# Kernel tuning notes

Hardware: AMD Instinct MI355X
Metric: run time of the kernel (lower is better)

## Reference

```python
import jax, jax.numpy as jnp
import numpy as np

N_NODES = 20000
N_EDGE_TYPES = 5
N_EDGES = 64000
IN_C, HID_C, OUT_C = 2048, 1024, 512


def setup_inputs() -> dict:
    key = jax.random.key(0)
    ks = jax.random.split(key, 12)
    s = 0.02
    return {
        "x": jax.random.normal(ks[0], (N_NODES, IN_C), jnp.float32),
        "edges": jax.random.randint(ks[1], (N_EDGE_TYPES, 2, N_EDGES), 0, N_NODES, dtype=jnp.int32),
        # SAGEConv weights, stacked over the 5 edge types. lin_l (neighbor agg, with bias), lin_r (root, no bias)
        "Wl1": jax.random.normal(ks[2], (N_EDGE_TYPES, HID_C, IN_C), jnp.float32) * s,
        "bl1": jnp.zeros((N_EDGE_TYPES, HID_C), jnp.float32),
        "Wr1": jax.random.normal(ks[3], (N_EDGE_TYPES, HID_C, IN_C), jnp.float32) * s,
        "Wl2": jax.random.normal(ks[4], (N_EDGE_TYPES, HID_C, HID_C), jnp.float32) * s,
        "bl2": jnp.zeros((N_EDGE_TYPES, HID_C), jnp.float32),
        "Wr2": jax.random.normal(ks[5], (N_EDGE_TYPES, HID_C, HID_C), jnp.float32) * s,
        "Wl3": jax.random.normal(ks[6], (N_EDGE_TYPES, OUT_C, HID_C), jnp.float32) * s,
        "bl3": jnp.zeros((N_EDGE_TYPES, OUT_C), jnp.float32),
        "Wr3": jax.random.normal(ks[7], (N_EDGE_TYPES, OUT_C, HID_C), jnp.float32) * s,
        "attn": jnp.ones((N_EDGE_TYPES,), jnp.float32),
    }


def sage_conv(h, src, dst, Wl, bl, Wr):
    # PyG SAGEConv(aggr='mean'): out = lin_l(mean_{j in N(i)} h_j) + lin_r(h_i)
    msg_sum = jax.ops.segment_sum(h[src], dst, num_segments=N_NODES)  # [N, C_in]
    deg = jax.ops.segment_sum(jnp.ones(src.shape, h.dtype), dst, num_segments=N_NODES)
    agg = msg_sum / jnp.maximum(deg, 1.0)[:, None]
    return agg @ Wl.T + bl + h @ Wr.T


def reference(x, edges, Wl1, bl1, Wr1, Wl2, bl2, Wr2, Wl3, bl3, Wr3, attn):
    outs = []
    for i in range(N_EDGE_TYPES):  # fixed small set of edge types
        src, dst = edges[i, 0], edges[i, 1]
        h = jax.nn.relu(sage_conv(x, src, dst, Wl1[i], bl1[i], Wr1[i]))
        h = jax.nn.relu(sage_conv(h, src, dst, Wl2[i], bl2[i], Wr2[i]))
        h = sage_conv(h, src, dst, Wl3[i], bl3[i], Wr3[i])  # no relu on final layer
        outs.append(h)
    w = jax.nn.softmax(attn)  # softmax-weighted combine over edge types
    combined = sum(w[i] * outs[i] for i in range(N_EDGE_TYPES))
    # F.normalize(p=2, dim=1, eps=1e-12)
    norm = jnp.linalg.norm(combined, axis=1, keepdims=True)
    return combined / jnp.maximum(norm, 1e-12)
```

## Files before the change

### kernel.cpp

```cpp
#include <hip/hip_runtime.h>
#include <hip/hip_bf16.h>
#include <stdint.h>

#define N_NODES   20000
#define MPAD      20224
#define N_TYPES   5
#define N_EDGES   64000
#define IN_C      2048
#define HID_C     1024
#define OUT_C     512

typedef __attribute__((ext_vector_type(8))) short short8;
typedef __attribute__((ext_vector_type(4))) float f32x4;

__device__ __forceinline__ unsigned short f2b(float f) {
  union { float f; uint32_t u; } c; c.f = f;
  uint32_t u = c.u;
  u += 0x7FFFu + ((u >> 16) & 1u);
  return (unsigned short)(u >> 16);
}
__device__ __forceinline__ float b2f(unsigned short h) {
  union { uint32_t u; float f; } c; c.u = ((uint32_t)h) << 16; return c.f;
}
__device__ __forceinline__ void gload_lds16(const void* g, void* l) {
  __builtin_amdgcn_global_load_lds((__attribute__((address_space(1))) void*)g,
                                   (__attribute__((address_space(3))) void*)l,
                                   16, 0, 0);
}

__global__ __launch_bounds__(64) void softmax5_k(const float* __restrict__ attn, float* __restrict__ w) {
  if (threadIdx.x == 0) {
    float m = attn[0];
    for (int i = 1; i < N_TYPES; ++i) m = fmaxf(m, attn[i]);
    float e[N_TYPES], s = 0.f;
    for (int i = 0; i < N_TYPES; ++i) { e[i] = expf(attn[i] - m); s += e[i]; }
    for (int i = 0; i < N_TYPES; ++i) w[i] = e[i] / s;
  }
}

__global__ __launch_bounds__(256) void zero_int_k(int* __restrict__ p, int n) {
  int i = blockIdx.x * 256 + threadIdx.x;
  if (i < n) p[i] = 0;
}

__global__ __launch_bounds__(256) void hist_k(const int* __restrict__ edges, int* __restrict__ deg) {
  int t = blockIdx.x * 256 + threadIdx.x;
  if (t < N_TYPES * N_EDGES) {
    int ty = t / N_EDGES, e = t - ty * N_EDGES;
    int dst = edges[ty * 2 * N_EDGES + N_EDGES + e];
    atomicAdd(&deg[ty * N_NODES + dst], 1);
  }
}

__global__ __launch_bounds__(256) void scan_k(const int* __restrict__ deg, int* __restrict__ rowptr,
                                              int* __restrict__ cursor) {
  int ty = blockIdx.x;
  const int* d = deg + ty * N_NODES;
  int* rp = rowptr + ty * (N_NODES + 1);
  int* cu = cursor + ty * N_NODES;
  __shared__ int sh[256];
  __shared__ int s_carry;
  int tid = threadIdx.x;
  if (tid == 0) s_carry = 0;
  __syncthreads();
  for (int base = 0; base < N_NODES; base += 256) {
    int i = base + tid;
    int v = (i < N_NODES) ? d[i] : 0;
    sh[tid] = v; __syncthreads();
    for (int off = 1; off < 256; off <<= 1) {
      int t2 = (tid >= off) ? sh[tid - off] : 0;
      __syncthreads();
      sh[tid] += t2;
      __syncthreads();
    }
    int incl = sh[tid];
    int c = s_carry;
    if (i < N_NODES) { rp[i] = c + incl - v; cu[i] = c + incl - v; }
    __syncthreads();
    if (tid == 255) s_carry = c + incl;
    __syncthreads();
  }
  if (tid == 0) rp[N_NODES] = s_carry;
}

__global__ __launch_bounds__(256) void scatter_k(const int* __restrict__ edges, int* __restrict__ cursor,
                                                 int* __restrict__ colidx) {
  int t = blockIdx.x * 256 + threadIdx.x;
  if (t < N_TYPES * N_EDGES) {
    int ty = t / N_EDGES, e = t - ty * N_EDGES;
    int src = edges[ty * 2 * N_EDGES + e];
    int dst = edges[ty * 2 * N_EDGES + N_EDGES + e];
    int pos = atomicAdd(&cursor[ty * N_NODES + dst], 1);
    colidx[ty * N_EDGES + pos] = src;
  }
}

__global__ __launch_bounds__(256) void cvt_x_k(const float* __restrict__ x, unsigned short* __restrict__ xb) {
  int i = blockIdx.x * 256 + threadIdx.x;
  int row = i >> 9;
  int c4 = (i & 511) << 2;
  if (row >= MPAD) return;
  ushort4 o;
  if (row < N_NODES) {
    float4 v = *(const float4*)(x + (size_t)row * IN_C + c4);
    o.x = f2b(v.x); o.y = f2b(v.y); o.z = f2b(v.z); o.w = f2b(v.w);
  } else { o.x = 0; o.y = 0; o.z = 0; o.w = 0; }
  *(ushort4*)(xb + (size_t)row * IN_C + c4) = o;
}

__global__ __launch_bounds__(256) void cvt_wcat_k(const float* __restrict__ s,
                                                  unsigned short* __restrict__ d,
                                                  int C, int K4, int rowoff) {
  int i = blockIdx.x * 256 + threadIdx.x;
  int total = N_TYPES * C * K4;
  if (i >= total) return;
  int k4 = i % K4;
  int rr = (i / K4) % C;
  int it = i / (C * K4);
  float4 v = ((const float4*)s)[i];
  ushort4 o; o.x = f2b(v.x); o.y = f2b(v.y); o.z = f2b(v.z); o.w = f2b(v.w);
  ((ushort4*)d)[((size_t)it * 2 * C + rowoff + rr) * K4 + k4] = o;
}

template<int NSIZE, int KSIZE>
__global__ __launch_bounds__(512, 2) void gemm_k(
    const unsigned short* __restrict__ Abase, size_t aS,
    const unsigned short* __restrict__ Wbase,
    unsigned short* __restrict__ PQ) {
  constexpr int NT = KSIZE / 32;
  constexpr int MT = MPAD / 256;
  constexpr int NB = NSIZE / 256;
  __shared__ unsigned short As[4][8192];
  __shared__ unsigned short Bs[4][8192];
  const int tid = threadIdx.x;
  const int lane = tid & 63;
  const int wave = tid >> 6;
  const int wm = wave >> 2, wn = wave & 3;

  const int nwg = gridDim.x;
  const int flat = blockIdx.x;
  const int q8 = nwg >> 3, r8 = nwg & 7;
  const int xcd = flat & 7, idx = flat >> 3;
  const int wg = (xcd < r8) ? (xcd * (q8 + 1) + idx) : (r8 * (q8 + 1) + (xcd - r8) * q8 + idx);
  const int itl = wg / (MT * NB);
  const int rem = wg % (MT * NB);
  const int row0 = (rem / NB) * 256;
  const int col0 = (rem % NB) * 256;

  const unsigned short* A = Abase + (size_t)itl * aS;
  const unsigned short* W = Wbase + (size_t)itl * NSIZE * KSIZE;

  const int sR = lane >> 3;
  const int su = (lane & 7) ^ (sR & 7);
  const int srow = 2 * sR + (su >> 2);
  const int selem = (su & 3) * 8;

  const int fr = lane & 15, k16 = lane >> 4;
  int aoff[8], boff[4];
#pragma unroll
  for (int m = 0; m < 8; ++m) {
    int r = wm * 128 + m * 16 + fr;
    aoff[m] = (((r >> 1) << 7) + ((r & 1) << 6) + (k16 << 4)) ^ (((r >> 1) & 7) << 4);
  }
#pragma unroll
  for (int n = 0; n < 4; ++n) {
    int r = wn * 64 + n * 16 + fr;
    boff[n] = (((r >> 1) << 7) + ((r & 1) << 6) + (k16 << 4)) ^ (((r >> 1) & 7) << 4);
  }

  auto stageA = [&](int t) {
    int s = t & 3; int kb = t * 32;
#pragma unroll
    for (int j = 0; j < 2; ++j) {
      int reg = wave + 8 * j;
      gload_lds16(A + (size_t)(row0 + reg * 16 + srow) * KSIZE + kb + selem, &As[s][reg * 512]);
    }
  };
  auto stageB = [&](int t) {
    int s = t & 3; int kb = t * 32;
#pragma unroll
    for (int j = 0; j < 2; ++j) {
      int reg = wave + 8 * j;
      gload_lds16(W + (size_t)(col0 + reg * 16 + srow) * KSIZE + kb + selem, &Bs[s][reg * 512]);
    }
  };

  f32x4 acc[8][4];
#pragma unroll
  for (int m = 0; m < 8; ++m)
#pragma unroll
    for (int n = 0; n < 4; ++n) acc[m][n] = (f32x4)(0.f);

  stageA(0); stageB(0);
  stageA(1); stageB(1);
  stageA(2); stageB(2);

  for (int t = 0; t < NT; ++t) {
    if (t < NT - 2)       asm volatile("s_waitcnt vmcnt(8)" ::: "memory");
    else if (t == NT - 2) asm volatile("s_waitcnt vmcnt(4)" ::: "memory");
    else                  asm volatile("s_waitcnt vmcnt(0)" ::: "memory");
    __builtin_amdgcn_s_barrier();
    __builtin_amdgcn_sched_barrier(0);
    const int slot = t & 3;
    const char* pa = (const char*)As[slot];
    const char* pb = (const char*)Bs[slot];
    short8 bf[4];
#pragma unroll
    for (int n = 0; n < 4; ++n) bf[n] = *(const short8*)(pb + boff[n]);
    short8 af[4];
#pragma unroll
    for (int m = 0; m < 4; ++m) af[m] = *(const short8*)(pa + aoff[m]);
    if (t + 3 < NT) stageA(t + 3);
    __builtin_amdgcn_s_setprio(1);
#pragma unroll
    for (int m = 0; m < 4; ++m)
#pragma unroll
      for (int n = 0; n < 4; ++n)
        acc[m][n] = __builtin_amdgcn_mfma_f32_16x16x32_bf16(af[m], bf[n], acc[m][n], 0, 0, 0);
    __builtin_amdgcn_s_setprio(0);
    __builtin_amdgcn_s_barrier();
    __builtin_amdgcn_sched_barrier(0);
#pragma unroll
    for (int m = 0; m < 4; ++m) af[m] = *(const short8*)(pa + aoff[m + 4]);
    if (t + 3 < NT) stageB(t + 3);
    __builtin_amdgcn_s_setprio(1);
#pragma unroll
    for (int m = 0; m < 4; ++m)
#pragma unroll
      for (int n = 0; n < 4; ++n)
        acc[m + 4][n] = __builtin_amdgcn_mfma_f32_16x16x32_bf16(af[m], bf[n], acc[m + 4][n], 0, 0, 0);
    __builtin_amdgcn_s_setprio(0);
  }

  const int erow = (lane >> 4) * 4;
  const int ecol = lane & 15;
  unsigned short* Op = PQ + (size_t)itl * MPAD * NSIZE;
#pragma unroll
  for (int m = 0; m < 8; ++m) {
#pragma unroll
    for (int n = 0; n < 4; ++n) {
      int gcol = col0 + wn * 64 + n * 16 + ecol;
#pragma unroll
      for (int r = 0; r < 4; ++r) {
        int grow = row0 + wm * 128 + m * 16 + erow + r;
        Op[(size_t)grow * NSIZE + gcol] = f2b(acc[m][n][r]);
      }
    }
  }
}

__global__ __launch_bounds__(256) void combine12_k(const unsigned short* __restrict__ PQ,
                                                   unsigned short* __restrict__ Hn,
                                                   const float* __restrict__ bl,
                                                   const int* __restrict__ rowptr,
                                                   const int* __restrict__ colidx, int it0) {
  constexpr int C = HID_C;
  int itl = blockIdx.x / MPAD;
  int node = blockIdx.x % MPAD;
  int it = it0 + itl;
  int tid = threadIdx.x;
  unsigned short* hp = Hn + ((size_t)itl * MPAD + node) * C + tid * 4;
  if (node >= N_NODES) {
    ushort4 z; z.x = 0; z.y = 0; z.z = 0; z.w = 0;
    *(ushort4*)hp = z;
    return;
  }
  const unsigned short* Pb = PQ + (size_t)itl * MPAD * 2 * C;
  const int* rp = rowptr + (size_t)it * (N_NODES + 1);
  const int* ci = colidx + (size_t)it * N_EDGES;
  int beg = rp[node], end = rp[node + 1];
  float a0 = 0.f, a1 = 0.f, a2 = 0.f, a3 = 0.f;
  for (int e = beg; e < end; ++e) {
    int src = ci[e];
    ushort4 u = *(const ushort4*)(Pb + (size_t)src * 2 * C + tid * 4);
    a0 += b2f(u.x); a1 += b2f(u.y); a2 += b2f(u.z); a3 += b2f(u.w);
  }
  float inv = (end > beg) ? 1.f / (float)(end - beg) : 0.f;
  a0 *= inv; a1 *= inv; a2 *= inv; a3 *= inv;
  ushort4 qv = *(const ushort4*)(Pb + (size_t)node * 2 * C + C + tid * 4);
  float4 bv = *(const float4*)(bl + (size_t)it * C + tid * 4);
  ushort4 o;
  o.x = f2b(fmaxf(a0 + b2f(qv.x) + bv.x, 0.f));
  o.y = f2b(fmaxf(a1 + b2f(qv.y) + bv.y, 0.f));
  o.z = f2b(fmaxf(a2 + b2f(qv.z) + bv.z, 0.f));
  o.w = f2b(fmaxf(a3 + b2f(qv.w) + bv.w, 0.f));
  *(ushort4*)hp = o;
}

__global__ __launch_bounds__(128) void combine3_k(const unsigned short* __restrict__ PQ,
                                                  const float* __restrict__ bl3,
                                                  const float* __restrict__ wsm,
                                                  const int* __restrict__ rowptr,
                                                  const int* __restrict__ colidx,
                                                  float* __restrict__ out, int it0, int nb, int acc) {
  int node = blockIdx.x;
  int tid = threadIdx.x;
  float s0 = 0.f, s1 = 0.f, s2 = 0.f, s3 = 0.f;
  for (int itl = 0; itl < nb; ++itl) {
    int it = it0 + itl;
    const unsigned short* Pb = PQ + (size_t)itl * MPAD * 1024;
    const int* rp = rowptr + (size_t)it * (N_NODES + 1);
    const int* ci = colidx + (size_t)it * N_EDGES;
    int beg = rp[node], end = rp[node + 1];
    float a0 = 0.f, a1 = 0.f, a2 = 0.f, a3 = 0.f;
    for (int e = beg; e < end; ++e) {
      int src = ci[e];
      ushort4 u = *(const ushort4*)(Pb + (size_t)src * 1024 + tid * 4);
      a0 += b2f(u.x); a1 += b2f(u.y); a2 += b2f(u.z); a3 += b2f(u.w);
    }
    float inv = (end > beg) ? 1.f / (float)(end - beg) : 0.f;
    ushort4 qv = *(const ushort4*)(Pb + (size_t)node * 1024 + 512 + tid * 4);
    float4 bv = *(const float4*)(bl3 + (size_t)it * OUT_C + tid * 4);
    float w = wsm[it];
    s0 += w * (a0 * inv + b2f(qv.x) + bv.x);
    s1 += w * (a1 * inv + b2f(qv.y) + bv.y);
    s2 += w * (a2 * inv + b2f(qv.z) + bv.z);
    s3 += w * (a3 * inv + b2f(qv.w) + bv.w);
  }
  float* op = out + (size_t)node * OUT_C + tid * 4;
  float4 cur = *(float4*)op;
  float4 nv;
  if (acc) { nv.x = cur.x + s0; nv.y = cur.y + s1; nv.z = cur.z + s2; nv.w = cur.w + s3; }
  else     { nv.x = s0; nv.y = s1; nv.z = s2; nv.w = s3; }
  *(float4*)op = nv;
}

__global__ __launch_bounds__(128) void l2norm_k(float* __restrict__ out) {
  int row = blockIdx.x;
  int tid = threadIdx.x;
  float4 v = ((float4*)(out + (size_t)row * OUT_C))[tid];
  float ss = v.x * v.x + v.y * v.y + v.z * v.z + v.w * v.w;
  for (int off = 32; off > 0; off >>= 1) ss += __shfl_down(ss, off);
  __shared__ float s2[2];
  if ((tid & 63) == 0) s2[tid >> 6] = ss;
  __syncthreads();
  float tot = s2[0] + s2[1];
  float inv = 1.f / fmaxf(sqrtf(tot), 1e-12f);
  v.x *= inv; v.y *= inv; v.z *= inv; v.w *= inv;
  ((float4*)(out + (size_t)row * OUT_C))[tid] = v;
}

extern "C" void kernel_launch(void* const* d_in, const int* in_sizes, int n_in,
                              void* d_out, int out_size, void* d_ws, size_t ws_size,
                              hipStream_t stream) {
  const float* x    = (const float*)d_in[0];
  const int*   edges = (const int*)d_in[1];
  const float* Wl1 = (const float*)d_in[2];
  const float* bl1 = (const float*)d_in[3];
  const float* Wr1 = (const float*)d_in[4];
  const float* Wl2 = (const float*)d_in[5];
  const float* bl2 = (const float*)d_in[6];
  const float* Wr2 = (const float*)d_in[7];
  const float* Wl3 = (const float*)d_in[8];
  const float* bl3 = (const float*)d_in[9];
  const float* Wr3 = (const float*)d_in[10];
  const float* attn = (const float*)d_in[11];
  float* out = (float*)d_out;

  char* ws = (char*)d_ws;
  size_t off = 0;
  auto alloc = [&](size_t bytes) -> char* {
    char* p = ws + off;
    off = (off + bytes + 255) & ~(size_t)255;
    return p;
  };
  float* wsm   = (float*)alloc(N_TYPES * 4);
  int* deg     = (int*)alloc((size_t)N_TYPES * N_NODES * 4);
  int* rowptr  = (int*)alloc((size_t)N_TYPES * (N_NODES + 1) * 4);
  int* cursor  = (int*)alloc((size_t)N_TYPES * N_NODES * 4);
  int* colidx  = (int*)alloc((size_t)N_TYPES * N_EDGES * 4);
  unsigned short* xb    = (unsigned short*)alloc((size_t)MPAD * IN_C * 2);
  unsigned short* wcat1 = (unsigned short*)alloc((size_t)N_TYPES * 2 * HID_C * IN_C * 2);
  unsigned short* wcat2 = (unsigned short*)alloc((size_t)N_TYPES * 2 * HID_C * HID_C * 2);
  unsigned short* wcat3 = (unsigned short*)alloc((size_t)N_TYPES * 2 * OUT_C * HID_C * 2);
  size_t persist = off;

  const size_t pqSlab = (size_t)MPAD * 2 * HID_C * 2;
  const size_t hSlab  = (size_t)MPAD * HID_C * 2;
  int nb = 1;
  for (int c = N_TYPES; c >= 1; --c) {
    size_t need = persist + (size_t)c * (pqSlab + hSlab) + 4096;
    if (need <= ws_size) { nb = c; break; }
  }
  unsigned short* PQ   = (unsigned short*)alloc((size_t)nb * pqSlab);
  unsigned short* hbuf = (unsigned short*)alloc((size_t)nb * hSlab);

  softmax5_k<<<1, 64, 0, stream>>>(attn, wsm);
  zero_int_k<<<(N_TYPES * N_NODES + 255) / 256, 256, 0, stream>>>(deg, N_TYPES * N_NODES);
  hist_k<<<(N_TYPES * N_EDGES + 255) / 256, 256, 0, stream>>>(edges, deg);
  scan_k<<<N_TYPES, 256, 0, stream>>>(deg, rowptr, cursor);
  scatter_k<<<(N_TYPES * N_EDGES + 255) / 256, 256, 0, stream>>>(edges, cursor, colidx);

  cvt_x_k<<<((size_t)MPAD * IN_C / 4 + 255) / 256, 256, 0, stream>>>(x, xb);
  {
    int t1 = N_TYPES * HID_C * (IN_C / 4);
    cvt_wcat_k<<<(t1 + 255) / 256, 256, 0, stream>>>(Wl1, wcat1, HID_C, IN_C / 4, 0);
    cvt_wcat_k<<<(t1 + 255) / 256, 256, 0, stream>>>(Wr1, wcat1, HID_C, IN_C / 4, HID_C);
    int t2 = N_TYPES * HID_C * (HID_C / 4);
    cvt_wcat_k<<<(t2 + 255) / 256, 256, 0, stream>>>(Wl2, wcat2, HID_C, HID_C / 4, 0);
    cvt_wcat_k<<<(t2 + 255) / 256, 256, 0, stream>>>(Wr2, wcat2, HID_C, HID_C / 4, HID_C);
    int t3 = N_TYPES * OUT_C * (HID_C / 4);
    cvt_wcat_k<<<(t3 + 255) / 256, 256, 0, stream>>>(Wl3, wcat3, OUT_C, HID_C / 4, 0);
    cvt_wcat_k<<<(t3 + 255) / 256, 256, 0, stream>>>(Wr3, wcat3, OUT_C, HID_C / 4, OUT_C);
  }

  const int MT = MPAD / 256;
  for (int g0 = 0; g0 < N_TYPES; g0 += nb) {
    int nbg = (N_TYPES - g0 < nb) ? (N_TYPES - g0) : nb;
    gemm_k<2 * HID_C, IN_C><<<nbg * MT * (2 * HID_C / 256), 512, 0, stream>>>(
        xb, 0, wcat1 + (size_t)g0 * 2 * HID_C * IN_C, PQ);
    combine12_k<<<nbg * MPAD, 256, 0, stream>>>(PQ, hbuf, bl1, rowptr, colidx, g0);
    gemm_k<2 * HID_C, HID_C><<<nbg * MT * (2 * HID_C / 256), 512, 0, stream>>>(
        hbuf, hSlab / 2, wcat2 + (size_t)g0 * 2 * HID_C * HID_C, PQ);
    combine12_k<<<nbg * MPAD, 256, 0, stream>>>(PQ, hbuf, bl2, rowptr, colidx, g0);
    gemm_k<2 * OUT_C, HID_C><<<nbg * MT * (2 * OUT_C / 256), 512, 0, stream>>>(
        hbuf, hSlab / 2, wcat3 + (size_t)g0 * 2 * OUT_C * HID_C, PQ);
    combine3_k<<<N_NODES, 128, 0, stream>>>(PQ, bl3, wsm, rowptr, colidx, out, g0, nbg,
                                            (g0 > 0) ? 1 : 0);
  }

  l2norm_k<<<N_NODES, 128, 0, stream>>>(out);
}
```

Before: 2.306 ms.

## Restructure GEMM mainloop to K=64 double-buffered tiles with four-phase schedule

The bf16 MFMA GEMM mainloop now steps K by 64 per iteration with two LDS buffers split into row halves, replacing the four-stage K=32 ring. Each iteration runs four compute phases over the quadrants of the wave's output tile. Between phases it issues the next A halves and the B halves two tiles ahead, which interleaves global-to-LDS loads with MFMA work. The LDS layout and XOR swizzle are rewritten for 128-byte rows. The aim is fewer barriers per unit of K and better load/compute overlap, at the cost of more barriers per iteration, more register use for fragments, and a more fragile wait-count schedule.

```diff
diff --git a/kernel.cpp b/kernel.cpp
--- a/kernel.cpp
+++ b/kernel.cpp
@@ -127,11 +127,11 @@
     const unsigned short* __restrict__ Abase, size_t aS,
     const unsigned short* __restrict__ Wbase,
     unsigned short* __restrict__ PQ) {
-  constexpr int NT = KSIZE / 32;
+  constexpr int NT = KSIZE / 64;
   constexpr int MT = MPAD / 256;
   constexpr int NB = NSIZE / 256;
-  __shared__ unsigned short As[4][8192];
-  __shared__ unsigned short Bs[4][8192];
+  __shared__ unsigned short As[2][2][8192];
+  __shared__ unsigned short Bs[2][2][8192];
   const int tid = threadIdx.x;
   const int lane = tid & 63;
   const int wave = tid >> 6;
@@ -150,38 +150,33 @@
   const unsigned short* A = Abase + (size_t)itl * aS;
   const unsigned short* W = Wbase + (size_t)itl * NSIZE * KSIZE;
 
-  const int sR = lane >> 3;
-  const int su = (lane & 7) ^ (sR & 7);
-  const int srow = 2 * sR + (su >> 2);
-  const int selem = (su & 3) * 8;
+  const int srow = lane >> 3;
+  const int skel = ((lane & 7) ^ (lane >> 3)) * 8;
 
   const int fr = lane & 15, k16 = lane >> 4;
+  const int swz = (k16 * 16) ^ ((fr & 7) << 4);
   int aoff[8], boff[4];
 #pragma unroll
-  for (int m = 0; m < 8; ++m) {
-    int r = wm * 128 + m * 16 + fr;
-    aoff[m] = (((r >> 1) << 7) + ((r & 1) << 6) + (k16 << 4)) ^ (((r >> 1) & 7) << 4);
-  }
-#pragma unroll
-  for (int n = 0; n < 4; ++n) {
-    int r = wn * 64 + n * 16 + fr;
-    boff[n] = (((r >> 1) << 7) + ((r & 1) << 6) + (k16 << 4)) ^ (((r >> 1) & 7) << 4);
-  }
-
-  auto stageA = [&](int t) {
-    int s = t & 3; int kb = t * 32;
+  for (int m = 0; m < 8; ++m) aoff[m] = (m * 16 + fr) * 128 + swz;
+#pragma unroll
+  for (int n = 0; n < 4; ++n) boff[n] = ((wn & 1) * 64 + n * 16 + fr) * 128 + swz;
+
+  auto stageAh = [&](int t, int half) {
+    int b = t & 1; int kb = t * 64;
 #pragma unroll
     for (int j = 0; j < 2; ++j) {
-      int reg = wave + 8 * j;
-      gload_lds16(A + (size_t)(row0 + reg * 16 + srow) * KSIZE + kb + selem, &As[s][reg * 512]);
+      int rb = (wave * 2 + j) * 8;
+      gload_lds16(A + (size_t)(row0 + half * 128 + rb + srow) * KSIZE + kb + skel,
+                  &As[b][half][(wave * 2 + j) * 512]);
     }
   };
-  auto stageB = [&](int t) {
-    int s = t & 3; int kb = t * 32;
+  auto stageBh = [&](int t, int half) {
+    int b = t & 1; int kb = t * 64;
 #pragma unroll
     for (int j = 0; j < 2; ++j) {
-      int reg = wave + 8 * j;
-      gload_lds16(W + (size_t)(col0 + reg * 16 + srow) * KSIZE + kb + selem, &Bs[s][reg * 512]);
+      int rb = (wave * 2 + j) * 8;
+      gload_lds16(W + (size_t)(col0 + half * 128 + rb + srow) * KSIZE + kb + skel,
+                  &Bs[b][half][(wave * 2 + j) * 512]);
     }
   };
 
@@ -191,45 +186,101 @@
 #pragma unroll
     for (int n = 0; n < 4; ++n) acc[m][n] = (f32x4)(0.f);
 
-  stageA(0); stageB(0);
-  stageA(1); stageB(1);
-  stageA(2); stageB(2);
+  stageAh(0, 0); stageAh(0, 1); stageBh(0, 0); stageBh(0, 1);
+  if (NT > 1) { stageBh(1, 0); stageBh(1, 1); }
+  asm volatile("s_waitcnt vmcnt(4)" ::: "memory");
+  __builtin_amdgcn_s_barrier();
+  __builtin_amdgcn_sched_barrier(0);
 
   for (int t = 0; t < NT; ++t) {
-    if (t < NT - 2)       asm volatile("s_waitcnt vmcnt(8)" ::: "memory");
-    else if (t == NT - 2) asm volatile("s_waitcnt vmcnt(4)" ::: "memory");
-    else                  asm volatile("s_waitcnt vmcnt(0)" ::: "memory");
-    __builtin_amdgcn_s_barrier();
+    const int b = t & 1;
+    const char* pa = (const char*)As[b][wm];
+    const char* pbl = (const char*)Bs[b][wn >> 1];
+    short8 afl[8], afh[8], bfl[4], bfh[4];
+
+#pragma unroll
+    for (int m = 0; m < 4; ++m) {
+      afl[m * 2 + 0] = *(const short8*)(pa + aoff[m]);
+      afl[m * 2 + 1] = *(const short8*)(pa + (aoff[m] ^ 64));
+    }
+#pragma unroll
+    for (int n = 0; n < 2; ++n) {
+      bfl[n * 2 + 0] = *(const short8*)(pbl + boff[n]);
+      bfl[n * 2 + 1] = *(const short8*)(pbl + (boff[n] ^ 64));
+    }
+    if (t + 1 < NT) stageAh(t + 1, 0);
+    __builtin_amdgcn_s_barrier();
+    asm volatile("s_waitcnt lgkmcnt(0)" ::: "memory");
     __builtin_amdgcn_sched_barrier(0);
-    const int slot = t & 3;
-    const char* pa = (const char*)As[slot];
-    const char* pb = (const char*)Bs[slot];
-    short8 bf[4];
-#pragma unroll
-    for (int n = 0; n < 4; ++n) bf[n] = *(const short8*)(pb + boff[n]);
-    short8 af[4];
-#pragma unroll
-    for (int m = 0; m < 4; ++m) af[m] = *(const short8*)(pa + aoff[m]);
-    if (t + 3 < NT) stageA(t + 3);
     __builtin_amdgcn_s_setprio(1);
 #pragma unroll
     for (int m = 0; m < 4; ++m)
 #pragma unroll
-      for (int n = 0; n < 4; ++n)
-        acc[m][n] = __builtin_amdgcn_mfma_f32_16x16x32_bf16(af[m], bf[n], acc[m][n], 0, 0, 0);
+      for (int n = 0; n < 2; ++n) {
+        acc[m][n] = __builtin_amdgcn_mfma_f32_16x16x32_bf16(afl[m * 2 + 0], bfl[n * 2 + 0], acc[m][n], 0, 0, 0);
+        acc[m][n] = __builtin_amdgcn_mfma_f32_16x16x32_bf16(afl[m * 2 + 1], bfl[n * 2 + 1], acc[m][n], 0, 0, 0);
+      }
     __builtin_amdgcn_s_setprio(0);
     __builtin_amdgcn_s_barrier();
+
+#pragma unroll
+    for (int n = 0; n < 2; ++n) {
+      bfh[n * 2 + 0] = *(const short8*)(pbl + boff[n + 2]);
+      bfh[n * 2 + 1] = *(const short8*)(pbl + (boff[n + 2] ^ 64));
+    }
+    if (t + 1 < NT) stageAh(t + 1, 1);
+    __builtin_amdgcn_s_barrier();
+    asm volatile("s_waitcnt lgkmcnt(0)" ::: "memory");
     __builtin_amdgcn_sched_barrier(0);
-#pragma unroll
-    for (int m = 0; m < 4; ++m) af[m] = *(const short8*)(pa + aoff[m + 4]);
-    if (t + 3 < NT) stageB(t + 3);
     __builtin_amdgcn_s_setprio(1);
 #pragma unroll
     for (int m = 0; m < 4; ++m)
 #pragma unroll
-      for (int n = 0; n < 4; ++n)
-        acc[m + 4][n] = __builtin_amdgcn_mfma_f32_16x16x32_bf16(af[m], bf[n], acc[m + 4][n], 0, 0, 0);
+      for (int n = 0; n < 2; ++n) {
+        acc[m][n + 2] = __builtin_amdgcn_mfma_f32_16x16x32_bf16(afl[m * 2 + 0], bfh[n * 2 + 0], acc[m][n + 2], 0, 0, 0);
+        acc[m][n + 2] = __builtin_amdgcn_mfma_f32_16x16x32_bf16(afl[m * 2 + 1], bfh[n * 2 + 1], acc[m][n + 2], 0, 0, 0);
+      }
     __builtin_amdgcn_s_setprio(0);
+    __builtin_amdgcn_s_barrier();
+
+#pragma unroll
+    for (int m = 0; m < 4; ++m) {
+      afh[m * 2 + 0] = *(const short8*)(pa + aoff[m + 4]);
+      afh[m * 2 + 1] = *(const short8*)(pa + (aoff[m + 4] ^ 64));
+    }
+    if (t + 2 < NT) stageBh(t + 2, 0);
+    __builtin_amdgcn_s_barrier();
+    asm volatile("s_waitcnt lgkmcnt(0)" ::: "memory");
+    __builtin_amdgcn_sched_barrier(0);
+    __builtin_amdgcn_s_setprio(1);
+#pragma unroll
+    for (int m = 0; m < 4; ++m)
+#pragma unroll
+      for (int n = 0; n < 2; ++n) {
+        acc[m + 4][n + 2] = __builtin_amdgcn_mfma_f32_16x16x32_bf16(afh[m * 2 + 0], bfh[n * 2 + 0], acc[m + 4][n + 2], 0, 0, 0);
+        acc[m + 4][n + 2] = __builtin_amdgcn_mfma_f32_16x16x32_bf16(afh[m * 2 + 1], bfh[n * 2 + 1], acc[m + 4][n + 2], 0, 0, 0);
+      }
+    __builtin_amdgcn_s_setprio(0);
+    __builtin_amdgcn_s_barrier();
+
+    if (t + 2 < NT) {
+      stageBh(t + 2, 1);
+      asm volatile("s_waitcnt vmcnt(4)" ::: "memory");
+    } else {
+      asm volatile("s_waitcnt vmcnt(0)" ::: "memory");
+    }
+    __builtin_amdgcn_s_barrier();
+    __builtin_amdgcn_sched_barrier(0);
+    __builtin_amdgcn_s_setprio(1);
+#pragma unroll
+    for (int m = 0; m < 4; ++m)
+#pragma unroll
+      for (int n = 0; n < 2; ++n) {
+        acc[m + 4][n] = __builtin_amdgcn_mfma_f32_16x16x32_bf16(afh[m * 2 + 0], bfl[n * 2 + 0], acc[m + 4][n], 0, 0, 0);
+        acc[m + 4][n] = __builtin_amdgcn_mfma_f32_16x16x32_bf16(afh[m * 2 + 1], bfl[n * 2 + 1], acc[m + 4][n], 0, 0, 0);
+      }
+    __builtin_amdgcn_s_setprio(0);
+    __builtin_amdgcn_s_barrier();
   }
 
   const int erow = (lane >> 4) * 4;
```

Measured after the change: 2.335 ms. About the same (+1.3%).
